# Kernel optimization log

Hardware: AMD Instinct MI355X
Metric: run time of the kernel (lower is better)

Reference implementation:

```python
import jax, jax.numpy as jnp
import numpy as np


def setup_inputs() -> dict:
    key = jax.random.key(0)
    ks = jax.random.split(key, 9)
    B, S, D, E, I = 4, 2048, 1024, 8, 2048
    sd = 1.0 / np.sqrt(D)
    si = 1.0 / np.sqrt(I)
    return {
        "hidden_states": jax.random.normal(ks[0], (B, S, D), dtype=jnp.float32),
        "gate_w": jax.random.normal(ks[1], (D, E), dtype=jnp.float32) * sd,
        "expert_gate_w": jax.random.normal(ks[2], (E, D, I), dtype=jnp.float32) * sd,
        "expert_up_w": jax.random.normal(ks[3], (E, D, I), dtype=jnp.float32) * sd,
        "expert_down_w": jax.random.normal(ks[4], (E, I, D), dtype=jnp.float32) * si,
        "shared_gate_proj_w": jax.random.normal(ks[5], (D, I), dtype=jnp.float32) * sd,
        "shared_up_w": jax.random.normal(ks[6], (D, I), dtype=jnp.float32) * sd,
        "shared_down_w": jax.random.normal(ks[7], (I, D), dtype=jnp.float32) * si,
        "shared_expert_gate_w": jax.random.normal(ks[8], (D, 1), dtype=jnp.float32) * sd,
        "top_k": 2,
    }


def reference(hidden_states, gate_w, expert_gate_w, expert_up_w, expert_down_w,
              shared_gate_proj_w, shared_up_w, shared_down_w, shared_expert_gate_w,
              top_k):
    B, S, D = hidden_states.shape
    E = gate_w.shape[1]
    x = hidden_states.reshape(-1, D)            # [T, D]
    T = x.shape[0]

    # Router: softmax in fp32, top-k, dense per-token per-expert combine weights.
    gate_vals = x @ gate_w                      # [T, E]
    probs = jax.nn.softmax(gate_vals.astype(jnp.float32), axis=-1)
    top_w, top_i = jax.lax.top_k(probs, top_k)  # [T, K]
    dense_w = jnp.zeros((T, E), dtype=jnp.float32)
    dense_w = dense_w.at[jnp.arange(T)[:, None], top_i].set(top_w)
    dense_w = dense_w.astype(x.dtype)           # zero for unselected experts

    # All experts as batched SwiGLU GEMMs (tokens with zero weight contribute 0).
    g = jnp.einsum('td,edi->eti', x, expert_gate_w)
    u = jnp.einsum('td,edi->eti', x, expert_up_w)
    y = jnp.einsum('eti,eid->etd', jax.nn.silu(g) * u, expert_down_w)  # [E, T, D]
    moe_out = jnp.einsum('etd,te->td', y, dense_w)                      # [T, D]

    # Shared expert with sigmoid gate.
    shared = (jax.nn.silu(x @ shared_gate_proj_w) * (x @ shared_up_w)) @ shared_down_w
    shared = jax.nn.sigmoid(x @ shared_expert_gate_w) * shared

    final = (moe_out + shared).reshape(B, S, D)
    return final, gate_vals
```

## Files before the change

kernel.cpp:

```cpp
#include <hip/hip_runtime.h>

typedef __bf16 bf16x8 __attribute__((ext_vector_type(8)));
typedef float f32x4 __attribute__((ext_vector_type(4)));
typedef float f4 __attribute__((ext_vector_type(4)));
typedef unsigned short us8 __attribute__((ext_vector_type(8)));

#define T_TOK 8192
#define DDIM 1024
#define NEXP 8
#define IDIM 2048
#define NCH 1024
#define RROWS 17408
#define ROWS_TOT (T_TOK + RROWS)

__device__ __forceinline__ unsigned short f2bf(float f) {
    unsigned u = __float_as_uint(f);
    u += 0x7fffu + ((u >> 16) & 1u);
    return (unsigned short)(u >> 16);
}

__global__ __launch_bounds__(256) void router_kernel(
    const float* __restrict__ x, const float* __restrict__ gate_w,
    const float* __restrict__ sgw, float* __restrict__ gate_out,
    float* __restrict__ wdense, float* __restrict__ sgout)
{
    __shared__ float lgw[DDIM * NEXP];
    __shared__ float lsg[DDIM];
    int tid = threadIdx.x;
    for (int i = tid; i < (DDIM * NEXP) / 4; i += 256)
        ((f4*)lgw)[i] = ((const f4*)gate_w)[i];
    for (int i = tid; i < DDIM / 4; i += 256)
        ((f4*)lsg)[i] = ((const f4*)sgw)[i];
    __syncthreads();

    int wid = tid >> 6, l = tid & 63;
    int t = blockIdx.x * 4 + wid;

    float acc[NEXP];
#pragma unroll
    for (int e = 0; e < NEXP; e++) acc[e] = 0.f;
    float accs = 0.f;
    const float* xr = x + (size_t)t * DDIM;
#pragma unroll
    for (int j = 0; j < 4; j++) {
        int d0 = j * 256 + l * 4;
        f4 xv = *(const f4*)(xr + d0);
#pragma unroll
        for (int c = 0; c < 4; c++) {
            float xd = xv[c];
            int d = d0 + c;
#pragma unroll
            for (int e = 0; e < NEXP; e++) acc[e] += xd * lgw[d * NEXP + e];
            accs += xd * lsg[d];
        }
    }
#pragma unroll
    for (int off = 32; off > 0; off >>= 1) {
#pragma unroll
        for (int e = 0; e < NEXP; e++) acc[e] += __shfl_xor(acc[e], off);
        accs += __shfl_xor(accs, off);
    }
    if (l == 0) {
        float m = acc[0];
        for (int e = 1; e < NEXP; e++) m = fmaxf(m, acc[e]);
        float p[NEXP], s = 0.f;
        for (int e = 0; e < NEXP; e++) { p[e] = __expf(acc[e] - m); s += p[e]; }
        float inv = 1.f / s;
        int i1 = 0; float b1 = p[0];
        for (int e = 1; e < NEXP; e++) if (p[e] > b1) { b1 = p[e]; i1 = e; }
        int i2 = -1; float b2 = -1.f;
        for (int e = 0; e < NEXP; e++) if (e != i1 && p[e] > b2) { b2 = p[e]; i2 = e; }
        for (int e = 0; e < NEXP; e++) {
            gate_out[(size_t)t * NEXP + e] = acc[e];
            float w = (e == i1) ? b1 * inv : (e == i2) ? b2 * inv : 0.f;
            wdense[(size_t)t * NEXP + e] = w;
        }
        sgout[t] = 1.f / (1.f + __expf(-accs));
    }
}

__global__ __launch_bounds__(256) void bucket_kernel(
    const float* __restrict__ wdense, int* __restrict__ list,
    float* __restrict__ wl, int* __restrict__ cnt,
    int* __restrict__ te, int* __restrict__ tp)
{
    int e = blockIdx.x;
    int tid = threadIdx.x, wid = tid >> 6, l = tid & 63;
    __shared__ int wsum[4];
    int base = 0;
    int* le = list + (size_t)e * T_TOK;
    float* we = wl + (size_t)e * T_TOK;
    for (int t0 = 0; t0 < T_TOK; t0 += 256) {
        int tok = t0 + tid;
        float w = wdense[(size_t)tok * NEXP + e];
        bool f = w > 0.f;
        unsigned long long m = __ballot(f);
        int lp = __popcll(m & ((1ull << l) - 1ull));
        if (l == 0) wsum[wid] = __popcll(m);
        __syncthreads();
        int woff = 0;
#pragma unroll
        for (int i = 0; i < 4; i++) if (i < wid) woff += wsum[i];
        int btot = wsum[0] + wsum[1] + wsum[2] + wsum[3];
        if (f) {
            int pos = base + woff + lp;
            le[pos] = tok; we[pos] = w;
            int slot = 0;
            for (int e2 = 0; e2 < e; e2++)
                slot += (wdense[(size_t)tok * NEXP + e2] > 0.f) ? 1 : 0;
            te[tok * 2 + slot] = e;
            tp[tok * 2 + slot] = pos;
        }
        base += btot;
        __syncthreads();
    }
    if (tid == 0) cnt[e] = base;
    int align = (base + 127) & ~127;
    for (int i = base + tid; i < align; i += 256) { le[i] = 0; we[i] = 0.f; }
}

__global__ void scan_kernel(const int* __restrict__ cnt, int* __restrict__ offs)
{
    if (threadIdx.x == 0) {
        int o = 0;
        for (int e = 0; e < NEXP; e++) { offs[e] = o; o += (cnt[e] + 127) & ~127; }
    }
}

__global__ __launch_bounds__(256) void cvt_kernel(
    const float* __restrict__ in, unsigned short* __restrict__ out, int n8)
{
    int i = blockIdx.x * 256 + threadIdx.x;
    if (i >= n8) return;
    const f4* p = (const f4*)in + (size_t)i * 2;
    f4 a = p[0], b = p[1];
    us8 o;
#pragma unroll
    for (int k = 0; k < 4; k++) { o[k] = f2bf(a[k]); o[4 + k] = f2bf(b[k]); }
    *((us8*)out + i) = o;
}

__global__ __launch_bounds__(256) void wcvt_gu_kernel(
    const float* __restrict__ egw, const float* __restrict__ euw,
    const float* __restrict__ sgp, const float* __restrict__ sup,
    unsigned short* __restrict__ pool, int c0)
{
    int j = blockIdx.y;
    int e = j >> 1, s = j & 1;
    const float* src = (e < 8) ? ((s ? euw : egw) + (size_t)e * DDIM * IDIM)
                               : (s ? sup : sgp);
    unsigned short* dst = pool + (size_t)j * NCH * DDIM;
    int tpc = NCH / 64;
    int tci = blockIdx.x % tpc, tri = blockIdx.x / tpc;
    int r0 = tri * 64;
    int cl0 = tci * 64;
    int cg0 = c0 + cl0;

    __shared__ unsigned short lds[64][72];
    int t = threadIdx.x;
    int tr = t >> 4, tcc = (t & 15) * 4;
#pragma unroll
    for (int jj = 0; jj < 4; jj++) {
        int r = tr + jj * 16;
        f4 v = *(const f4*)(src + (size_t)(r0 + r) * IDIM + cg0 + tcc);
#pragma unroll
        for (int k = 0; k < 4; k++) lds[r][tcc + k] = f2bf(v[k]);
    }
    __syncthreads();
    int orow = t >> 2, ss = t & 3;
    us8 v0, v1;
#pragma unroll
    for (int i = 0; i < 8; i++) {
        v0[i] = lds[ss * 16 + i][orow];
        v1[i] = lds[ss * 16 + 8 + i][orow];
    }
    unsigned short* op = dst + (size_t)(cl0 + orow) * DDIM + r0 + ss * 16;
    *(us8*)op = v0; *(us8*)(op + 8) = v1;
}

__global__ __launch_bounds__(256) void wcvt_d_kernel(
    const float* __restrict__ edw, const float* __restrict__ sdw,
    unsigned short* __restrict__ pool)
{
    int j = blockIdx.y;
    const float* src = (j < 8) ? edw + (size_t)j * IDIM * DDIM : sdw;
    unsigned short* dst = pool + (size_t)j * DDIM * IDIM;
    int tpc = DDIM / 64;
    int tci = blockIdx.x % tpc, tri = blockIdx.x / tpc;
    int rg0 = tri * 64;
    int cg0 = tci * 64;

    __shared__ unsigned short lds[64][72];
    int t = threadIdx.x;
    int tr = t >> 4, tcc = (t & 15) * 4;
#pragma unroll
    for (int jj = 0; jj < 4; jj++) {
        int r = tr + jj * 16;
        f4 v = *(const f4*)(src + (size_t)(rg0 + r) * DDIM + cg0 + tcc);
#pragma unroll
        for (int k = 0; k < 4; k++) lds[r][tcc + k] = f2bf(v[k]);
    }
    __syncthreads();
    int orow = t >> 2, ss = t & 3;
    us8 v0, v1;
#pragma unroll
    for (int i = 0; i < 8; i++) {
        v0[i] = lds[ss * 16 + i][orow];
        v1[i] = lds[ss * 16 + 8 + i][orow];
    }
    unsigned short* op = dst + (size_t)(cg0 + orow) * IDIM + rg0 + ss * 16;
    *(us8*)op = v0; *(us8*)(op + 8) = v1;
}

__device__ __forceinline__ void stage_tile(
    const unsigned short* __restrict__ g, int row0, int ldk, int k0,
    unsigned short* lds, int wid, int lane)
{
#pragma unroll
    for (int j = 0; j < 2; j++) {
        int c = wid + j * 4;
        int seg = c * 64 + lane;
        int row = seg >> 2, ks = seg & 3;
        const unsigned short* gp = g + (size_t)(row0 + row) * ldk + k0 + ks * 8;
        __builtin_amdgcn_global_load_lds(
            (const __attribute__((address_space(1))) void*)gp,
            (__attribute__((address_space(3))) void*)(lds + c * 512),
            16, 0, 0);
    }
}

__global__ __launch_bounds__(256, 2) void gemm_gateup(
    const unsigned short* __restrict__ A, const unsigned short* __restrict__ pool,
    unsigned short* __restrict__ H, const int* __restrict__ listb,
    const int* __restrict__ cnt, const int* __restrict__ offs, int c0)
{
    int z = blockIdx.z;
    const unsigned short *Bg, *Bu; const int* lst; int count, rowb;
    if (z == 0) {
        Bg = pool + (size_t)16 * NCH * DDIM; Bu = pool + (size_t)17 * NCH * DDIM;
        lst = nullptr; count = T_TOK; rowb = 0;
    } else {
        int e = z - 1;
        Bg = pool + (size_t)(e * 2) * NCH * DDIM; Bu = pool + (size_t)(e * 2 + 1) * NCH * DDIM;
        lst = listb + (size_t)e * T_TOK; count = cnt[e]; rowb = T_TOK + offs[e];
    }
    int flat = blockIdx.y * 8 + blockIdx.x;
    int nt = flat & 7, mt = flat >> 3;
    int m0 = mt * 128, n0 = nt * 128;
    if (m0 >= count) return;
    const int K = DDIM;

    __shared__ unsigned short As[128 * 32], Bgs[128 * 32], Bus[128 * 32];
    int tid = threadIdx.x, wid = tid >> 6, l = tid & 63;
    int wm = wid >> 1, wn = wid & 1;
    int lr = l & 15, kg = l >> 4;

    int seg0 = wid * 64 + l, seg1 = (wid + 4) * 64 + l;
    int ra0 = seg0 >> 2, ka0 = seg0 & 3;
    int ra1 = seg1 >> 2, ka1 = seg1 & 3;
    int ga0 = lst ? lst[m0 + ra0] : (m0 + ra0);
    int ga1 = lst ? lst[m0 + ra1] : (m0 + ra1);
    const unsigned short* pa0 = A + (size_t)ga0 * K + ka0 * 8;
    const unsigned short* pa1 = A + (size_t)ga1 * K + ka1 * 8;

    f32x4 zero = {0.f, 0.f, 0.f, 0.f};
    f32x4 accg[4][4], accu[4][4];
#pragma unroll
    for (int m = 0; m < 4; m++)
#pragma unroll
        for (int n = 0; n < 4; n++) { accg[m][n] = zero; accu[m][n] = zero; }

    for (int k0 = 0; k0 < K; k0 += 32) {
        __builtin_amdgcn_global_load_lds(
            (const __attribute__((address_space(1))) void*)(pa0 + k0),
            (__attribute__((address_space(3))) void*)(As + wid * 512), 16, 0, 0);
        __builtin_amdgcn_global_load_lds(
            (const __attribute__((address_space(1))) void*)(pa1 + k0),
            (__attribute__((address_space(3))) void*)(As + (wid + 4) * 512), 16, 0, 0);
        stage_tile(Bg, n0, K, k0, Bgs, wid, l);
        stage_tile(Bu, n0, K, k0, Bus, wid, l);
        __syncthreads();
        bf16x8 a[4], bg[4], bu[4];
#pragma unroll
        for (int m = 0; m < 4; m++)
            a[m] = *(const bf16x8*)(As + ((wm * 64 + m * 16 + lr) * 32 + kg * 8));
#pragma unroll
        for (int n = 0; n < 4; n++) {
            bg[n] = *(const bf16x8*)(Bgs + ((wn * 64 + n * 16 + lr) * 32 + kg * 8));
            bu[n] = *(const bf16x8*)(Bus + ((wn * 64 + n * 16 + lr) * 32 + kg * 8));
        }
#pragma unroll
        for (int m = 0; m < 4; m++)
#pragma unroll
            for (int n = 0; n < 4; n++) {
                accg[m][n] = __builtin_amdgcn_mfma_f32_16x16x32_bf16(a[m], bg[n], accg[m][n], 0, 0, 0);
                accu[m][n] = __builtin_amdgcn_mfma_f32_16x16x32_bf16(a[m], bu[n], accu[m][n], 0, 0, 0);
            }
        __syncthreads();
    }

#pragma unroll
    for (int m = 0; m < 4; m++) {
        int row = rowb + m0 + wm * 64 + m * 16 + kg * 4;
#pragma unroll
        for (int n = 0; n < 4; n++) {
            int col = c0 + n0 + wn * 64 + n * 16 + lr;
#pragma unroll
            for (int r = 0; r < 4; r++) {
                float g = accg[m][n][r], u = accu[m][n][r];
                float hv = g * (1.f / (1.f + __expf(-g))) * u;
                H[(size_t)(row + r) * IDIM + col] = f2bf(hv);
            }
        }
    }
}

__global__ __launch_bounds__(256, 2) void gemm_down(
    const unsigned short* __restrict__ H, const unsigned short* __restrict__ pool,
    unsigned short* __restrict__ Y,
    const float* __restrict__ wlb, const float* __restrict__ sgo,
    const int* __restrict__ cnt, const int* __restrict__ offs)
{
    int z = blockIdx.z;
    const unsigned short* B; const float* coef; int count, rowb;
    if (z == 0) {
        B = pool + (size_t)8 * DDIM * IDIM;
        coef = sgo; count = T_TOK; rowb = 0;
    } else {
        int e = z - 1;
        B = pool + (size_t)e * DDIM * IDIM;
        coef = wlb + (size_t)e * T_TOK;
        count = cnt[e]; rowb = T_TOK + offs[e];
    }
    int flat = blockIdx.y * 8 + blockIdx.x;
    int nt = flat & 7, mt = flat >> 3;
    int m0 = mt * 128, n0 = nt * 128;
    if (m0 >= count) return;
    const unsigned short* Arows = H + (size_t)rowb * IDIM;

    __shared__ unsigned short As[128 * 32], Bs[128 * 32];
    int tid = threadIdx.x, wid = tid >> 6, l = tid & 63;
    int wm = wid >> 1, wn = wid & 1;
    int lr = l & 15, kg = l >> 4;

    f32x4 zero = {0.f, 0.f, 0.f, 0.f};
    f32x4 acc[4][4];
#pragma unroll
    for (int m = 0; m < 4; m++)
#pragma unroll
        for (int n = 0; n < 4; n++) acc[m][n] = zero;

    for (int k0 = 0; k0 < IDIM; k0 += 32) {
        stage_tile(Arows, m0, IDIM, k0, As, wid, l);
        stage_tile(B, n0, IDIM, k0, Bs, wid, l);
        __syncthreads();
        bf16x8 a[4], b[4];
#pragma unroll
        for (int m = 0; m < 4; m++)
            a[m] = *(const bf16x8*)(As + ((wm * 64 + m * 16 + lr) * 32 + kg * 8));
#pragma unroll
        for (int n = 0; n < 4; n++)
            b[n] = *(const bf16x8*)(Bs + ((wn * 64 + n * 16 + lr) * 32 + kg * 8));
#pragma unroll
        for (int m = 0; m < 4; m++)
#pragma unroll
            for (int n = 0; n < 4; n++)
                acc[m][n] = __builtin_amdgcn_mfma_f32_16x16x32_bf16(a[m], b[n], acc[m][n], 0, 0, 0);
        __syncthreads();
    }

#pragma unroll
    for (int m = 0; m < 4; m++) {
        int rloc = m0 + wm * 64 + m * 16 + kg * 4;
        float cf[4];
#pragma unroll
        for (int r = 0; r < 4; r++) cf[r] = coef[rloc + r];
#pragma unroll
        for (int n = 0; n < 4; n++) {
            int col = n0 + wn * 64 + n * 16 + lr;
#pragma unroll
            for (int r = 0; r < 4; r++)
                Y[(size_t)(rowb + rloc + r) * DDIM + col] = f2bf(cf[r] * acc[m][n][r]);
        }
    }
}

__global__ __launch_bounds__(256) void combine_kernel(
    const unsigned short* __restrict__ Y, const int* __restrict__ te,
    const int* __restrict__ tp, const int* __restrict__ offs,
    float* __restrict__ out)
{
    int t = blockIdx.x * 2 + (threadIdx.x >> 7);
    int c = (threadIdx.x & 127) * 8;
    int e0 = te[2 * t], e1 = te[2 * t + 1];
    size_t r0 = (size_t)T_TOK + offs[e0] + tp[2 * t];
    size_t r1 = (size_t)T_TOK + offs[e1] + tp[2 * t + 1];

    us8 vs = *(const us8*)(Y + (size_t)t * DDIM + c);
    us8 v0 = *(const us8*)(Y + r0 * DDIM + c);
    us8 v1 = *(const us8*)(Y + r1 * DDIM + c);
    f4 o0, o1;
#pragma unroll
    for (int k = 0; k < 4; k++) {
        o0[k] = __uint_as_float((unsigned)vs[k] << 16)
              + __uint_as_float((unsigned)v0[k] << 16)
              + __uint_as_float((unsigned)v1[k] << 16);
        o1[k] = __uint_as_float((unsigned)vs[4 + k] << 16)
              + __uint_as_float((unsigned)v0[4 + k] << 16)
              + __uint_as_float((unsigned)v1[4 + k] << 16);
    }
    float* op = out + (size_t)t * DDIM + c;
    *(f4*)op = o0;
    *(f4*)(op + 4) = o1;
}

extern "C" void kernel_launch(void* const* d_in, const int* in_sizes, int n_in,
                              void* d_out, int out_size, void* d_ws, size_t ws_size,
                              hipStream_t stream)
{
    const float* x   = (const float*)d_in[0];
    const float* gw  = (const float*)d_in[1];
    const float* egw = (const float*)d_in[2];
    const float* euw = (const float*)d_in[3];
    const float* edw = (const float*)d_in[4];
    const float* sgp = (const float*)d_in[5];
    const float* sup = (const float*)d_in[6];
    const float* sdw = (const float*)d_in[7];
    const float* seg = (const float*)d_in[8];

    float* out0 = (float*)d_out;
    float* gate_out = out0 + (size_t)T_TOK * DDIM;

    char* ws = (char*)d_ws;
    auto take = [&](size_t bytes) { char* p = ws; ws += (bytes + 255) & ~(size_t)255; return p; };
    unsigned short* xb   = (unsigned short*)take((size_t)T_TOK * DDIM * 2);
    float* wdense = (float*)take((size_t)T_TOK * NEXP * 4);
    float* sgo    = (float*)take((size_t)T_TOK * 4);
    int*   list   = (int*)take((size_t)NEXP * T_TOK * 4);
    float* wl     = (float*)take((size_t)NEXP * T_TOK * 4);
    int*   cnt    = (int*)take(256);
    int*   offs   = (int*)take(256);
    int*   te     = (int*)take((size_t)T_TOK * 2 * 4);
    int*   tp     = (int*)take((size_t)T_TOK * 2 * 4);
    unsigned short* pool = (unsigned short*)take((size_t)18 * NCH * DDIM * 2);
    unsigned short* H    = (unsigned short*)take((size_t)ROWS_TOT * IDIM * 2);
    unsigned short* Y    = (unsigned short*)take((size_t)ROWS_TOT * DDIM * 2);

    router_kernel<<<T_TOK / 4, 256, 0, stream>>>(x, gw, seg, gate_out, wdense, sgo);
    bucket_kernel<<<NEXP, 256, 0, stream>>>(wdense, list, wl, cnt, te, tp);
    scan_kernel<<<1, 64, 0, stream>>>(cnt, offs);
    cvt_kernel<<<(T_TOK * DDIM / 8) / 256, 256, 0, stream>>>(x, xb, T_TOK * DDIM / 8);

    for (int c = 0; c < 2; c++) {
        int c0 = c * NCH;
        wcvt_gu_kernel<<<dim3((NCH / 64) * 16, 18), 256, 0, stream>>>(
            egw, euw, sgp, sup, pool, c0);
        gemm_gateup<<<dim3(8, 64, 9), 256, 0, stream>>>(
            xb, pool, H, list, cnt, offs, c0);
    }

    wcvt_d_kernel<<<dim3((IDIM / 64) * 16, 9), 256, 0, stream>>>(edw, sdw, pool);
    gemm_down<<<dim3(8, 64, 9), 256, 0, stream>>>(H, pool, Y, wl, sgo, cnt, offs);

    combine_kernel<<<T_TOK / 2, 256, 0, stream>>>(Y, te, tp, offs, out0);
}
```

Before: 590.8 us.

## Rewrite MoE GEMMs with 8-wave 256-row tiles, double-buffered swizzled LDS pipeline

Both the gate/up and down GEMMs move to 512-thread blocks with 256-row M tiles (down also uses 256-wide N) and K steps of 64. They use a two-stage double-buffered global-to-LDS pipeline with explicit vmcnt waits, XOR-swizzled LDS layout to avoid bank conflicts, interleaved MFMA phases with s_setprio, and split barriers. Expert bucket padding grows to 256 rows and stores are guarded to the 128-aligned count. The intent is to overlap memory with compute, raise arithmetic intensity, and cut LDS conflicts. The cost is more register and LDS pressure (64 KB per buffer pair) and wasted work on padded rows.

```diff
diff --git a/kernel.cpp b/kernel.cpp
--- a/kernel.cpp
+++ b/kernel.cpp
@@ -18,6 +18,10 @@
     u += 0x7fffu + ((u >> 16) & 1u);
     return (unsigned short)(u >> 16);
 }
+
+#define GLDS(src, dst) __builtin_amdgcn_global_load_lds( \
+    (const __attribute__((address_space(1))) void*)(src), \
+    (__attribute__((address_space(3))) void*)(dst), 16, 0, 0)
 
 __global__ __launch_bounds__(256) void router_kernel(
     const float* __restrict__ x, const float* __restrict__ gate_w,
@@ -115,7 +119,7 @@
         __syncthreads();
     }
     if (tid == 0) cnt[e] = base;
-    int align = (base + 127) & ~127;
+    int align = (base + 255) & ~255;
     for (int i = base + tid; i < align; i += 256) { le[i] = 0; we[i] = 0.f; }
 }
 
@@ -212,24 +216,7 @@
     *(us8*)op = v0; *(us8*)(op + 8) = v1;
 }
 
-__device__ __forceinline__ void stage_tile(
-    const unsigned short* __restrict__ g, int row0, int ldk, int k0,
-    unsigned short* lds, int wid, int lane)
-{
-#pragma unroll
-    for (int j = 0; j < 2; j++) {
-        int c = wid + j * 4;
-        int seg = c * 64 + lane;
-        int row = seg >> 2, ks = seg & 3;
-        const unsigned short* gp = g + (size_t)(row0 + row) * ldk + k0 + ks * 8;
-        __builtin_amdgcn_global_load_lds(
-            (const __attribute__((address_space(1))) void*)gp,
-            (__attribute__((address_space(3))) void*)(lds + c * 512),
-            16, 0, 0);
-    }
-}
-
-__global__ __launch_bounds__(256, 2) void gemm_gateup(
+__global__ __launch_bounds__(512, 2) void gemm_gateup8(
     const unsigned short* __restrict__ A, const unsigned short* __restrict__ pool,
     unsigned short* __restrict__ H, const int* __restrict__ listb,
     const int* __restrict__ cnt, const int* __restrict__ offs, int c0)
@@ -244,24 +231,60 @@
         Bg = pool + (size_t)(e * 2) * NCH * DDIM; Bu = pool + (size_t)(e * 2 + 1) * NCH * DDIM;
         lst = listb + (size_t)e * T_TOK; count = cnt[e]; rowb = T_TOK + offs[e];
     }
-    int flat = blockIdx.y * 8 + blockIdx.x;
-    int nt = flat & 7, mt = flat >> 3;
-    int m0 = mt * 128, n0 = nt * 128;
+    int m0 = blockIdx.y * 256, n0 = blockIdx.x * 128;
     if (m0 >= count) return;
-    const int K = DDIM;
-
-    __shared__ unsigned short As[128 * 32], Bgs[128 * 32], Bus[128 * 32];
+    int climit = (count + 127) & ~127;
+    const int NT = DDIM / 64;
+
+    __shared__ unsigned short lds[2][32768];
+
     int tid = threadIdx.x, wid = tid >> 6, l = tid & 63;
     int wm = wid >> 1, wn = wid & 1;
-    int lr = l & 15, kg = l >> 4;
-
-    int seg0 = wid * 64 + l, seg1 = (wid + 4) * 64 + l;
-    int ra0 = seg0 >> 2, ka0 = seg0 & 3;
-    int ra1 = seg1 >> 2, ka1 = seg1 & 3;
-    int ga0 = lst ? lst[m0 + ra0] : (m0 + ra0);
-    int ga1 = lst ? lst[m0 + ra1] : (m0 + ra1);
-    const unsigned short* pa0 = A + (size_t)ga0 * K + ka0 * 8;
-    const unsigned short* pa1 = A + (size_t)ga1 * K + ka1 * 8;
+    int lr = l & 15, lkg = l >> 4;
+
+    int sb = tid & 7, sr = tid >> 3;
+    int sk = (sb ^ (sr & 7)) << 3;
+    const unsigned short* pa[2][2];
+#pragma unroll
+    for (int h = 0; h < 2; h++)
+#pragma unroll
+        for (int j = 0; j < 2; j++) {
+            int rr = m0 + h * 128 + j * 64 + sr;
+            int ga = lst ? lst[rr] : rr;
+            pa[h][j] = A + (size_t)ga * DDIM + sk;
+        }
+    const unsigned short* pbg = Bg + (size_t)(n0 + sr) * DDIM + sk;
+    const unsigned short* pbu = Bu + (size_t)(n0 + sr) * DDIM + sk;
+
+#define GU_ST_A(sbuf, h, t) { \
+    GLDS(pa[h][0] + (t) * 64, (sbuf) + (h) * 8192 + tid * 8); \
+    GLDS(pa[h][1] + (t) * 64, (sbuf) + (h) * 8192 + 4096 + tid * 8); }
+#define GU_ST_BG(sbuf, t) { \
+    GLDS(pbg + (t) * 64, (sbuf) + 16384 + tid * 8); \
+    GLDS(pbg + (size_t)64 * DDIM + (t) * 64, (sbuf) + 16384 + 4096 + tid * 8); }
+#define GU_ST_BU(sbuf, t) { \
+    GLDS(pbu + (t) * 64, (sbuf) + 24576 + tid * 8); \
+    GLDS(pbu + (size_t)64 * DDIM + (t) * 64, (sbuf) + 24576 + 4096 + tid * 8); }
+
+    {
+        unsigned short* s0 = &lds[0][0];
+        GU_ST_A(s0, 0, 0); GU_ST_A(s0, 1, 0); GU_ST_BG(s0, 0); GU_ST_BU(s0, 0);
+        unsigned short* s1 = &lds[1][0];
+        GU_ST_A(s1, 0, 1); GU_ST_A(s1, 1, 1); GU_ST_BG(s1, 1); GU_ST_BU(s1, 1);
+    }
+
+    int xorc = (lr & 7) << 3;
+    int kx0 = (lkg * 8) ^ xorc;
+    int kx1 = (32 + lkg * 8) ^ xorc;
+    int aoff[4], boff[4];
+#pragma unroll
+    for (int mf = 0; mf < 4; mf++) {
+        int r = wm * 64 + mf * 16 + lr;
+        aoff[mf] = (r >> 7) * 8192 + (r & 127) * 64;
+    }
+#pragma unroll
+    for (int nf = 0; nf < 4; nf++)
+        boff[nf] = 16384 + (wn * 64 + nf * 16 + lr) * 64;
 
     f32x4 zero = {0.f, 0.f, 0.f, 0.f};
     f32x4 accg[4][4], accu[4][4];
@@ -270,52 +293,115 @@
 #pragma unroll
         for (int n = 0; n < 4; n++) { accg[m][n] = zero; accu[m][n] = zero; }
 
-    for (int k0 = 0; k0 < K; k0 += 32) {
-        __builtin_amdgcn_global_load_lds(
-            (const __attribute__((address_space(1))) void*)(pa0 + k0),
-            (__attribute__((address_space(3))) void*)(As + wid * 512), 16, 0, 0);
-        __builtin_amdgcn_global_load_lds(
-            (const __attribute__((address_space(1))) void*)(pa1 + k0),
-            (__attribute__((address_space(3))) void*)(As + (wid + 4) * 512), 16, 0, 0);
-        stage_tile(Bg, n0, K, k0, Bgs, wid, l);
-        stage_tile(Bu, n0, K, k0, Bus, wid, l);
-        __syncthreads();
-        bf16x8 a[4], bg[4], bu[4];
-#pragma unroll
-        for (int m = 0; m < 4; m++)
-            a[m] = *(const bf16x8*)(As + ((wm * 64 + m * 16 + lr) * 32 + kg * 8));
-#pragma unroll
-        for (int n = 0; n < 4; n++) {
-            bg[n] = *(const bf16x8*)(Bgs + ((wn * 64 + n * 16 + lr) * 32 + kg * 8));
-            bu[n] = *(const bf16x8*)(Bus + ((wn * 64 + n * 16 + lr) * 32 + kg * 8));
-        }
-#pragma unroll
-        for (int m = 0; m < 4; m++)
-#pragma unroll
-            for (int n = 0; n < 4; n++) {
-                accg[m][n] = __builtin_amdgcn_mfma_f32_16x16x32_bf16(a[m], bg[n], accg[m][n], 0, 0, 0);
-                accu[m][n] = __builtin_amdgcn_mfma_f32_16x16x32_bf16(a[m], bu[n], accu[m][n], 0, 0, 0);
+    bf16x8 a[2][2], bg[4][2], bu[4][2];
+
+#pragma unroll 1
+    for (int t = 0; t < NT; t++) {
+        const unsigned short* cb = &lds[t & 1][0];
+        unsigned short* sbuf = &lds[t & 1][0];
+        bool stg = (t + 2 < NT);
+
+        if (t == NT - 1) { asm volatile("s_waitcnt vmcnt(0)" ::: "memory"); }
+        else             { asm volatile("s_waitcnt vmcnt(8)" ::: "memory"); }
+        __builtin_amdgcn_s_barrier();
+#pragma unroll
+        for (int mf = 0; mf < 2; mf++) {
+            a[mf][0] = *(const bf16x8*)(cb + aoff[mf] + kx0);
+            a[mf][1] = *(const bf16x8*)(cb + aoff[mf] + kx1);
+        }
+#pragma unroll
+        for (int nf = 0; nf < 2; nf++) {
+            bg[nf][0] = *(const bf16x8*)(cb + boff[nf] + kx0);
+            bg[nf][1] = *(const bf16x8*)(cb + boff[nf] + kx1);
+            bu[nf][0] = *(const bf16x8*)(cb + boff[nf] + 8192 + kx0);
+            bu[nf][1] = *(const bf16x8*)(cb + boff[nf] + 8192 + kx1);
+        }
+        __builtin_amdgcn_s_setprio(1);
+#pragma unroll
+        for (int kh = 0; kh < 2; kh++)
+#pragma unroll
+            for (int mf = 0; mf < 2; mf++)
+#pragma unroll
+                for (int nf = 0; nf < 2; nf++) {
+                    accg[mf][nf] = __builtin_amdgcn_mfma_f32_16x16x32_bf16(a[mf][kh], bg[nf][kh], accg[mf][nf], 0, 0, 0);
+                    accu[mf][nf] = __builtin_amdgcn_mfma_f32_16x16x32_bf16(a[mf][kh], bu[nf][kh], accu[mf][nf], 0, 0, 0);
+                }
+        __builtin_amdgcn_s_setprio(0);
+
+        __builtin_amdgcn_s_barrier();
+#pragma unroll
+        for (int nf = 2; nf < 4; nf++) {
+            bg[nf][0] = *(const bf16x8*)(cb + boff[nf] + kx0);
+            bg[nf][1] = *(const bf16x8*)(cb + boff[nf] + kx1);
+            bu[nf][0] = *(const bf16x8*)(cb + boff[nf] + 8192 + kx0);
+            bu[nf][1] = *(const bf16x8*)(cb + boff[nf] + 8192 + kx1);
+        }
+        __builtin_amdgcn_s_setprio(1);
+#pragma unroll
+        for (int kh = 0; kh < 2; kh++)
+#pragma unroll
+            for (int mf = 0; mf < 2; mf++)
+#pragma unroll
+                for (int nf = 2; nf < 4; nf++) {
+                    accg[mf][nf] = __builtin_amdgcn_mfma_f32_16x16x32_bf16(a[mf][kh], bg[nf][kh], accg[mf][nf], 0, 0, 0);
+                    accu[mf][nf] = __builtin_amdgcn_mfma_f32_16x16x32_bf16(a[mf][kh], bu[nf][kh], accu[mf][nf], 0, 0, 0);
+                }
+        __builtin_amdgcn_s_setprio(0);
+
+        __builtin_amdgcn_s_barrier();
+#pragma unroll
+        for (int mf = 0; mf < 2; mf++) {
+            a[mf][0] = *(const bf16x8*)(cb + aoff[2 + mf] + kx0);
+            a[mf][1] = *(const bf16x8*)(cb + aoff[2 + mf] + kx1);
+        }
+        if (stg) { GU_ST_BG(sbuf, t + 2); }
+        __builtin_amdgcn_s_setprio(1);
+#pragma unroll
+        for (int kh = 0; kh < 2; kh++)
+#pragma unroll
+            for (int mf = 0; mf < 2; mf++)
+#pragma unroll
+                for (int nf = 0; nf < 2; nf++) {
+                    accg[2 + mf][nf] = __builtin_amdgcn_mfma_f32_16x16x32_bf16(a[mf][kh], bg[nf][kh], accg[2 + mf][nf], 0, 0, 0);
+                    accu[2 + mf][nf] = __builtin_amdgcn_mfma_f32_16x16x32_bf16(a[mf][kh], bu[nf][kh], accu[2 + mf][nf], 0, 0, 0);
+                }
+        __builtin_amdgcn_s_setprio(0);
+
+        __builtin_amdgcn_s_barrier();
+        if (stg) { GU_ST_BU(sbuf, t + 2); GU_ST_A(sbuf, 0, t + 2); GU_ST_A(sbuf, 1, t + 2); }
+        __builtin_amdgcn_s_setprio(1);
+#pragma unroll
+        for (int kh = 0; kh < 2; kh++)
+#pragma unroll
+            for (int mf = 0; mf < 2; mf++)
+#pragma unroll
+                for (int nf = 2; nf < 4; nf++) {
+                    accg[2 + mf][nf] = __builtin_amdgcn_mfma_f32_16x16x32_bf16(a[mf][kh], bg[nf][kh], accg[2 + mf][nf], 0, 0, 0);
+                    accu[2 + mf][nf] = __builtin_amdgcn_mfma_f32_16x16x32_bf16(a[mf][kh], bu[nf][kh], accu[2 + mf][nf], 0, 0, 0);
+                }
+        __builtin_amdgcn_s_setprio(0);
+    }
+
+#pragma unroll
+    for (int mf = 0; mf < 4; mf++) {
+        int rbase = m0 + wm * 64 + mf * 16 + lkg * 4;
+#pragma unroll
+        for (int nf = 0; nf < 4; nf++) {
+            int col = c0 + n0 + wn * 64 + nf * 16 + lr;
+#pragma unroll
+            for (int r = 0; r < 4; r++) {
+                int rloc = rbase + r;
+                if (rloc < climit) {
+                    float g = accg[mf][nf][r], u = accu[mf][nf][r];
+                    float hv = g * (1.f / (1.f + __expf(-g))) * u;
+                    H[(size_t)(rowb + rloc) * IDIM + col] = f2bf(hv);
+                }
             }
-        __syncthreads();
-    }
-
-#pragma unroll
-    for (int m = 0; m < 4; m++) {
-        int row = rowb + m0 + wm * 64 + m * 16 + kg * 4;
-#pragma unroll
-        for (int n = 0; n < 4; n++) {
-            int col = c0 + n0 + wn * 64 + n * 16 + lr;
-#pragma unroll
-            for (int r = 0; r < 4; r++) {
-                float g = accg[m][n][r], u = accu[m][n][r];
-                float hv = g * (1.f / (1.f + __expf(-g))) * u;
-                H[(size_t)(row + r) * IDIM + col] = f2bf(hv);
-            }
-        }
-    }
-}
-
-__global__ __launch_bounds__(256, 2) void gemm_down(
+        }
+    }
+}
+
+__global__ __launch_bounds__(512, 2) void gemm_down8(
     const unsigned short* __restrict__ H, const unsigned short* __restrict__ pool,
     unsigned short* __restrict__ Y,
     const float* __restrict__ wlb, const float* __restrict__ sgo,
@@ -332,55 +418,149 @@
         coef = wlb + (size_t)e * T_TOK;
         count = cnt[e]; rowb = T_TOK + offs[e];
     }
-    int flat = blockIdx.y * 8 + blockIdx.x;
-    int nt = flat & 7, mt = flat >> 3;
-    int m0 = mt * 128, n0 = nt * 128;
+    int m0 = blockIdx.y * 256, n0 = blockIdx.x * 256;
     if (m0 >= count) return;
-    const unsigned short* Arows = H + (size_t)rowb * IDIM;
-
-    __shared__ unsigned short As[128 * 32], Bs[128 * 32];
+    int climit = (count + 127) & ~127;
+    const int NT = IDIM / 64;
+
+    __shared__ unsigned short lds[2][32768];
+
     int tid = threadIdx.x, wid = tid >> 6, l = tid & 63;
-    int wm = wid >> 1, wn = wid & 1;
-    int lr = l & 15, kg = l >> 4;
+    int wm = wid >> 2, wn = wid & 3;
+    int lr = l & 15, lkg = l >> 4;
+
+    int sb = tid & 7, sr = tid >> 3;
+    int sk = (sb ^ (sr & 7)) << 3;
+    const unsigned short* pah = H + (size_t)(rowb + m0 + sr) * IDIM + sk;
+    const unsigned short* pb  = B + (size_t)(n0 + sr) * IDIM + sk;
+
+#define DN_ST_A(sbuf, h, t) { \
+    GLDS(pah + (size_t)((h) * 128) * IDIM + (t) * 64, (sbuf) + (h) * 8192 + tid * 8); \
+    GLDS(pah + (size_t)((h) * 128 + 64) * IDIM + (t) * 64, (sbuf) + (h) * 8192 + 4096 + tid * 8); }
+#define DN_ST_B(sbuf, h, t) { \
+    GLDS(pb + (size_t)((h) * 128) * IDIM + (t) * 64, (sbuf) + 16384 + (h) * 8192 + tid * 8); \
+    GLDS(pb + (size_t)((h) * 128 + 64) * IDIM + (t) * 64, (sbuf) + 16384 + (h) * 8192 + 4096 + tid * 8); }
+
+    {
+        unsigned short* s0 = &lds[0][0];
+        DN_ST_A(s0, 0, 0); DN_ST_A(s0, 1, 0); DN_ST_B(s0, 0, 0); DN_ST_B(s0, 1, 0);
+        unsigned short* s1 = &lds[1][0];
+        DN_ST_A(s1, 0, 1); DN_ST_A(s1, 1, 1); DN_ST_B(s1, 0, 1); DN_ST_B(s1, 1, 1);
+    }
+
+    int xorc = (lr & 7) << 3;
+    int kx0 = (lkg * 8) ^ xorc;
+    int kx1 = (32 + lkg * 8) ^ xorc;
+    int aoff[8], boff[4];
+#pragma unroll
+    for (int mf = 0; mf < 8; mf++)
+        aoff[mf] = wm * 8192 + (mf * 16 + lr) * 64;
+#pragma unroll
+    for (int nf = 0; nf < 4; nf++)
+        boff[nf] = 16384 + (wn * 64 + nf * 16 + lr) * 64;
 
     f32x4 zero = {0.f, 0.f, 0.f, 0.f};
-    f32x4 acc[4][4];
-#pragma unroll
-    for (int m = 0; m < 4; m++)
+    f32x4 acc[8][4];
+#pragma unroll
+    for (int m = 0; m < 8; m++)
 #pragma unroll
         for (int n = 0; n < 4; n++) acc[m][n] = zero;
 
-    for (int k0 = 0; k0 < IDIM; k0 += 32) {
-        stage_tile(Arows, m0, IDIM, k0, As, wid, l);
-        stage_tile(B, n0, IDIM, k0, Bs, wid, l);
-        __syncthreads();
-        bf16x8 a[4], b[4];
-#pragma unroll
-        for (int m = 0; m < 4; m++)
-            a[m] = *(const bf16x8*)(As + ((wm * 64 + m * 16 + lr) * 32 + kg * 8));
-#pragma unroll
-        for (int n = 0; n < 4; n++)
-            b[n] = *(const bf16x8*)(Bs + ((wn * 64 + n * 16 + lr) * 32 + kg * 8));
-#pragma unroll
-        for (int m = 0; m < 4; m++)
-#pragma unroll
-            for (int n = 0; n < 4; n++)
-                acc[m][n] = __builtin_amdgcn_mfma_f32_16x16x32_bf16(a[m], b[n], acc[m][n], 0, 0, 0);
-        __syncthreads();
-    }
-
-#pragma unroll
-    for (int m = 0; m < 4; m++) {
-        int rloc = m0 + wm * 64 + m * 16 + kg * 4;
+    bf16x8 a[4][2], b[4][2];
+
+#pragma unroll 1
+    for (int t = 0; t < NT; t++) {
+        const unsigned short* cb = &lds[t & 1][0];
+        unsigned short* sbuf = &lds[t & 1][0];
+        bool stg = (t + 2 < NT);
+
+        if (t == NT - 1) { asm volatile("s_waitcnt vmcnt(0)" ::: "memory"); }
+        else             { asm volatile("s_waitcnt vmcnt(8)" ::: "memory"); }
+        __builtin_amdgcn_s_barrier();
+#pragma unroll
+        for (int mf = 0; mf < 4; mf++) {
+            a[mf][0] = *(const bf16x8*)(cb + aoff[mf] + kx0);
+            a[mf][1] = *(const bf16x8*)(cb + aoff[mf] + kx1);
+        }
+#pragma unroll
+        for (int nf = 0; nf < 2; nf++) {
+            b[nf][0] = *(const bf16x8*)(cb + boff[nf] + kx0);
+            b[nf][1] = *(const bf16x8*)(cb + boff[nf] + kx1);
+        }
+        __builtin_amdgcn_s_setprio(1);
+#pragma unroll
+        for (int kh = 0; kh < 2; kh++)
+#pragma unroll
+            for (int mf = 0; mf < 4; mf++)
+#pragma unroll
+                for (int nf = 0; nf < 2; nf++)
+                    acc[mf][nf] = __builtin_amdgcn_mfma_f32_16x16x32_bf16(a[mf][kh], b[nf][kh], acc[mf][nf], 0, 0, 0);
+        __builtin_amdgcn_s_setprio(0);
+
+        __builtin_amdgcn_s_barrier();
+#pragma unroll
+        for (int nf = 2; nf < 4; nf++) {
+            b[nf][0] = *(const bf16x8*)(cb + boff[nf] + kx0);
+            b[nf][1] = *(const bf16x8*)(cb + boff[nf] + kx1);
+        }
+        __builtin_amdgcn_s_setprio(1);
+#pragma unroll
+        for (int kh = 0; kh < 2; kh++)
+#pragma unroll
+            for (int mf = 0; mf < 4; mf++)
+#pragma unroll
+                for (int nf = 2; nf < 4; nf++)
+                    acc[mf][nf] = __builtin_amdgcn_mfma_f32_16x16x32_bf16(a[mf][kh], b[nf][kh], acc[mf][nf], 0, 0, 0);
+        __builtin_amdgcn_s_setprio(0);
+
+        __builtin_amdgcn_s_barrier();
+#pragma unroll
+        for (int mf = 0; mf < 4; mf++) {
+            a[mf][0] = *(const bf16x8*)(cb + aoff[4 + mf] + kx0);
+            a[mf][1] = *(const bf16x8*)(cb + aoff[4 + mf] + kx1);
+        }
+        if (stg) { DN_ST_B(sbuf, 0, t + 2); }
+        __builtin_amdgcn_s_setprio(1);
+#pragma unroll
+        for (int kh = 0; kh < 2; kh++)
+#pragma unroll
+            for (int mf = 0; mf < 4; mf++)
+#pragma unroll
+                for (int nf = 0; nf < 2; nf++)
+                    acc[4 + mf][nf] = __builtin_amdgcn_mfma_f32_16x16x32_bf16(a[mf][kh], b[nf][kh], acc[4 + mf][nf], 0, 0, 0);
+        __builtin_amdgcn_s_setprio(0);
+
+        __builtin_amdgcn_s_barrier();
+        if (stg) { DN_ST_B(sbuf, 1, t + 2); DN_ST_A(sbuf, 0, t + 2); DN_ST_A(sbuf, 1, t + 2); }
+        __builtin_amdgcn_s_setprio(1);
+#pragma unroll
+        for (int kh = 0; kh < 2; kh++)
+#pragma unroll
+            for (int mf = 0; mf < 4; mf++)
+#pragma unroll
+                for (int nf = 2; nf < 4; nf++)
+                    acc[4 + mf][nf] = __builtin_amdgcn_mfma_f32_16x16x32_bf16(a[mf][kh], b[nf][kh], acc[4 + mf][nf], 0, 0, 0);
+        __builtin_amdgcn_s_setprio(0);
+    }
+
+#pragma unroll
+    for (int mf = 0; mf < 8; mf++) {
+        int rbase = m0 + wm * 128 + mf * 16 + lkg * 4;
         float cf[4];
 #pragma unroll
-        for (int r = 0; r < 4; r++) cf[r] = coef[rloc + r];
-#pragma unroll
-        for (int n = 0; n < 4; n++) {
-            int col = n0 + wn * 64 + n * 16 + lr;
-#pragma unroll
-            for (int r = 0; r < 4; r++)
-                Y[(size_t)(rowb + rloc + r) * DDIM + col] = f2bf(cf[r] * acc[m][n][r]);
+        for (int r = 0; r < 4; r++) {
+            int rloc = rbase + r;
+            cf[r] = (rloc < climit) ? coef[rloc] : 0.f;
+        }
+#pragma unroll
+        for (int nf = 0; nf < 4; nf++) {
+            int col = n0 + wn * 64 + nf * 16 + lr;
+#pragma unroll
+            for (int r = 0; r < 4; r++) {
+                int rloc = rbase + r;
+                if (rloc < climit)
+                    Y[(size_t)(rowb + rloc) * DDIM + col] = f2bf(cf[r] * acc[mf][nf][r]);
+            }
         }
     }
 }
@@ -455,12 +635,13 @@
         int c0 = c * NCH;
         wcvt_gu_kernel<<<dim3((NCH / 64) * 16, 18), 256, 0, stream>>>(
             egw, euw, sgp, sup, pool, c0);
-        gemm_gateup<<<dim3(8, 64, 9), 256, 0, stream>>>(
+        gemm_gateup8<<<dim3(NCH / 128, T_TOK / 256, 9), 512, 0, stream>>>(
             xb, pool, H, list, cnt, offs, c0);
     }
 
     wcvt_d_kernel<<<dim3((IDIM / 64) * 16, 9), 256, 0, stream>>>(edw, sdw, pool);
-    gemm_down<<<dim3(8, 64, 9), 256, 0, stream>>>(H, pool, Y, wl, sgo, cnt, offs);
+    gemm_down8<<<dim3(DDIM / 256, T_TOK / 256, 9), 512, 0, stream>>>(
+        H, pool, Y, wl, sgo, cnt, offs);
 
     combine_kernel<<<T_TOK / 2, 256, 0, stream>>>(Y, te, tp, offs, out0);
 }
```

After: 552.0 us. -6.6%, faster.

## Double-buffer GEMM LDS staging with XOR-swizzled layout and prefetch depth two

Applied to the files above, without the earlier changes.

Rewrites both expert GEMMs to use a two-stage LDS ring filled by direct global-to-LDS loads issued two K-tiles ahead, synchronized with explicit vmcnt waits and raw barriers. It also applies an XOR swizzle to the K offset so the bf16x8 LDS reads avoid bank conflicts. Launch bounds for the down GEMM go up to 4 blocks per CU, and the bucket padding changes from 128 to 256 rows with guarded epilogue stores. The goal is to overlap global loads with MFMA work and cut LDS conflicts, at the cost of more shared memory per block and fragile hand-managed wait counts.

```diff
diff --git a/kernel.cpp b/kernel.cpp
--- a/kernel.cpp
+++ b/kernel.cpp
@@ -18,6 +18,10 @@
     u += 0x7fffu + ((u >> 16) & 1u);
     return (unsigned short)(u >> 16);
 }
+
+#define GLDS(src, dst) __builtin_amdgcn_global_load_lds( \
+    (const __attribute__((address_space(1))) void*)(src), \
+    (__attribute__((address_space(3))) void*)(dst), 16, 0, 0)
 
 __global__ __launch_bounds__(256) void router_kernel(
     const float* __restrict__ x, const float* __restrict__ gate_w,
@@ -115,7 +119,7 @@
         __syncthreads();
     }
     if (tid == 0) cnt[e] = base;
-    int align = (base + 127) & ~127;
+    int align = (base + 255) & ~255;
     for (int i = base + tid; i < align; i += 256) { le[i] = 0; we[i] = 0.f; }
 }
 
@@ -212,24 +216,8 @@
     *(us8*)op = v0; *(us8*)(op + 8) = v1;
 }
 
-__device__ __forceinline__ void stage_tile(
-    const unsigned short* __restrict__ g, int row0, int ldk, int k0,
-    unsigned short* lds, int wid, int lane)
-{
-#pragma unroll
-    for (int j = 0; j < 2; j++) {
-        int c = wid + j * 4;
-        int seg = c * 64 + lane;
-        int row = seg >> 2, ks = seg & 3;
-        const unsigned short* gp = g + (size_t)(row0 + row) * ldk + k0 + ks * 8;
-        __builtin_amdgcn_global_load_lds(
-            (const __attribute__((address_space(1))) void*)gp,
-            (__attribute__((address_space(3))) void*)(lds + c * 512),
-            16, 0, 0);
-    }
-}
-
-__global__ __launch_bounds__(256, 2) void gemm_gateup(
+
+__global__ __launch_bounds__(256, 2) void gemm_gateup8(
     const unsigned short* __restrict__ A, const unsigned short* __restrict__ pool,
     unsigned short* __restrict__ H, const int* __restrict__ listb,
     const int* __restrict__ cnt, const int* __restrict__ offs, int c0)
@@ -244,24 +232,49 @@
         Bg = pool + (size_t)(e * 2) * NCH * DDIM; Bu = pool + (size_t)(e * 2 + 1) * NCH * DDIM;
         lst = listb + (size_t)e * T_TOK; count = cnt[e]; rowb = T_TOK + offs[e];
     }
-    int flat = blockIdx.y * 8 + blockIdx.x;
-    int nt = flat & 7, mt = flat >> 3;
-    int m0 = mt * 128, n0 = nt * 128;
+    int m0 = blockIdx.y * 128, n0 = blockIdx.x * 128;
     if (m0 >= count) return;
-    const int K = DDIM;
-
-    __shared__ unsigned short As[128 * 32], Bgs[128 * 32], Bus[128 * 32];
+    int climit = (count + 127) & ~127;
+    const int NT = DDIM / 32;
+
+    __shared__ unsigned short lds[2][12288];
+
     int tid = threadIdx.x, wid = tid >> 6, l = tid & 63;
     int wm = wid >> 1, wn = wid & 1;
-    int lr = l & 15, kg = l >> 4;
-
-    int seg0 = wid * 64 + l, seg1 = (wid + 4) * 64 + l;
-    int ra0 = seg0 >> 2, ka0 = seg0 & 3;
-    int ra1 = seg1 >> 2, ka1 = seg1 & 3;
-    int ga0 = lst ? lst[m0 + ra0] : (m0 + ra0);
-    int ga1 = lst ? lst[m0 + ra1] : (m0 + ra1);
-    const unsigned short* pa0 = A + (size_t)ga0 * K + ka0 * 8;
-    const unsigned short* pa1 = A + (size_t)ga1 * K + ka1 * 8;
+    int lr = l & 15, lkg = l >> 4;
+
+    int srow0 = tid >> 2, srow1 = 64 + (tid >> 2);
+    int skof = (((tid & 3) ^ ((tid >> 3) & 3))) << 3;
+    int ga0 = lst ? lst[m0 + srow0] : (m0 + srow0);
+    int ga1 = lst ? lst[m0 + srow1] : (m0 + srow1);
+    const unsigned short* paA0 = A + (size_t)ga0 * DDIM + skof;
+    const unsigned short* paA1 = A + (size_t)ga1 * DDIM + skof;
+    const unsigned short* pbg0 = Bg + (size_t)(n0 + srow0) * DDIM + skof;
+    const unsigned short* pbg1 = Bg + (size_t)(n0 + srow1) * DDIM + skof;
+    const unsigned short* pbu0 = Bu + (size_t)(n0 + srow0) * DDIM + skof;
+    const unsigned short* pbu1 = Bu + (size_t)(n0 + srow1) * DDIM + skof;
+
+#define GU_ST(sbuf, t) { \
+    GLDS(paA0 + (t) * 32, (sbuf) + tid * 8); \
+    GLDS(paA1 + (t) * 32, (sbuf) + 2048 + tid * 8); \
+    GLDS(pbg0 + (t) * 32, (sbuf) + 4096 + tid * 8); \
+    GLDS(pbg1 + (t) * 32, (sbuf) + 6144 + tid * 8); \
+    GLDS(pbu0 + (t) * 32, (sbuf) + 8192 + tid * 8); \
+    GLDS(pbu1 + (t) * 32, (sbuf) + 10240 + tid * 8); }
+
+    GU_ST(&lds[0][0], 0);
+    GU_ST(&lds[1][0], 1);
+    asm volatile("s_waitcnt vmcnt(6)" ::: "memory");
+    __builtin_amdgcn_s_barrier();
+
+    int kx = ((lkg) ^ ((lr >> 1) & 3)) << 3;
+    int aoff[4], goff[4], uoff[4];
+#pragma unroll
+    for (int f = 0; f < 4; f++) {
+        aoff[f] = (wm * 64 + f * 16 + lr) * 32 + kx;
+        goff[f] = 4096 + (wn * 64 + f * 16 + lr) * 32 + kx;
+        uoff[f] = 8192 + (wn * 64 + f * 16 + lr) * 32 + kx;
+    }
 
     f32x4 zero = {0.f, 0.f, 0.f, 0.f};
     f32x4 accg[4][4], accu[4][4];
@@ -270,52 +283,55 @@
 #pragma unroll
         for (int n = 0; n < 4; n++) { accg[m][n] = zero; accu[m][n] = zero; }
 
-    for (int k0 = 0; k0 < K; k0 += 32) {
-        __builtin_amdgcn_global_load_lds(
-            (const __attribute__((address_space(1))) void*)(pa0 + k0),
-            (__attribute__((address_space(3))) void*)(As + wid * 512), 16, 0, 0);
-        __builtin_amdgcn_global_load_lds(
-            (const __attribute__((address_space(1))) void*)(pa1 + k0),
-            (__attribute__((address_space(3))) void*)(As + (wid + 4) * 512), 16, 0, 0);
-        stage_tile(Bg, n0, K, k0, Bgs, wid, l);
-        stage_tile(Bu, n0, K, k0, Bus, wid, l);
-        __syncthreads();
+    for (int t = 0; t < NT; t++) {
+        const unsigned short* cb = &lds[t & 1][0];
+        unsigned short* sbuf = &lds[t & 1][0];
+        bool stg = (t + 2 < NT);
+
         bf16x8 a[4], bg[4], bu[4];
 #pragma unroll
-        for (int m = 0; m < 4; m++)
-            a[m] = *(const bf16x8*)(As + ((wm * 64 + m * 16 + lr) * 32 + kg * 8));
-#pragma unroll
-        for (int n = 0; n < 4; n++) {
-            bg[n] = *(const bf16x8*)(Bgs + ((wn * 64 + n * 16 + lr) * 32 + kg * 8));
-            bu[n] = *(const bf16x8*)(Bus + ((wn * 64 + n * 16 + lr) * 32 + kg * 8));
-        }
-#pragma unroll
-        for (int m = 0; m < 4; m++)
-#pragma unroll
-            for (int n = 0; n < 4; n++) {
-                accg[m][n] = __builtin_amdgcn_mfma_f32_16x16x32_bf16(a[m], bg[n], accg[m][n], 0, 0, 0);
-                accu[m][n] = __builtin_amdgcn_mfma_f32_16x16x32_bf16(a[m], bu[n], accu[m][n], 0, 0, 0);
+        for (int f = 0; f < 4; f++) {
+            a[f]  = *(const bf16x8*)(cb + aoff[f]);
+            bg[f] = *(const bf16x8*)(cb + goff[f]);
+            bu[f] = *(const bf16x8*)(cb + uoff[f]);
+        }
+#pragma unroll
+        for (int mf = 0; mf < 4; mf++)
+#pragma unroll
+            for (int nf = 0; nf < 4; nf++) {
+                accg[mf][nf] = __builtin_amdgcn_mfma_f32_16x16x32_bf16(a[mf], bg[nf], accg[mf][nf], 0, 0, 0);
+                accu[mf][nf] = __builtin_amdgcn_mfma_f32_16x16x32_bf16(a[mf], bu[nf], accu[mf][nf], 0, 0, 0);
             }
-        __syncthreads();
-    }
-
-#pragma unroll
-    for (int m = 0; m < 4; m++) {
-        int row = rowb + m0 + wm * 64 + m * 16 + kg * 4;
-#pragma unroll
-        for (int n = 0; n < 4; n++) {
-            int col = c0 + n0 + wn * 64 + n * 16 + lr;
+        __builtin_amdgcn_s_barrier();
+        if (stg) {
+            GU_ST(sbuf, t + 2);
+            asm volatile("s_waitcnt vmcnt(6)" ::: "memory");
+        } else {
+            asm volatile("s_waitcnt vmcnt(0)" ::: "memory");
+        }
+        __builtin_amdgcn_s_barrier();
+    }
+
+#pragma unroll
+    for (int mf = 0; mf < 4; mf++) {
+        int rbase = m0 + wm * 64 + mf * 16 + lkg * 4;
+#pragma unroll
+        for (int nf = 0; nf < 4; nf++) {
+            int col = c0 + n0 + wn * 64 + nf * 16 + lr;
 #pragma unroll
             for (int r = 0; r < 4; r++) {
-                float g = accg[m][n][r], u = accu[m][n][r];
-                float hv = g * (1.f / (1.f + __expf(-g))) * u;
-                H[(size_t)(row + r) * IDIM + col] = f2bf(hv);
+                int rloc = rbase + r;
+                if (rloc < climit) {
+                    float g = accg[mf][nf][r], u = accu[mf][nf][r];
+                    float hv = g * (1.f / (1.f + __expf(-g))) * u;
+                    H[(size_t)(rowb + rloc) * IDIM + col] = f2bf(hv);
+                }
             }
         }
     }
 }
 
-__global__ __launch_bounds__(256, 2) void gemm_down(
+__global__ __launch_bounds__(256, 4) void gemm_down8(
     const unsigned short* __restrict__ H, const unsigned short* __restrict__ pool,
     unsigned short* __restrict__ Y,
     const float* __restrict__ wlb, const float* __restrict__ sgo,
@@ -332,16 +348,42 @@
         coef = wlb + (size_t)e * T_TOK;
         count = cnt[e]; rowb = T_TOK + offs[e];
     }
-    int flat = blockIdx.y * 8 + blockIdx.x;
-    int nt = flat & 7, mt = flat >> 3;
-    int m0 = mt * 128, n0 = nt * 128;
+    int m0 = blockIdx.y * 128, n0 = blockIdx.x * 128;
     if (m0 >= count) return;
-    const unsigned short* Arows = H + (size_t)rowb * IDIM;
-
-    __shared__ unsigned short As[128 * 32], Bs[128 * 32];
+    int climit = (count + 127) & ~127;
+    const int NT = IDIM / 32;
+
+    __shared__ unsigned short lds[2][8192];
+
     int tid = threadIdx.x, wid = tid >> 6, l = tid & 63;
     int wm = wid >> 1, wn = wid & 1;
-    int lr = l & 15, kg = l >> 4;
+    int lr = l & 15, lkg = l >> 4;
+
+    int srow0 = tid >> 2, srow1 = 64 + (tid >> 2);
+    int skof = (((tid & 3) ^ ((tid >> 3) & 3))) << 3;
+    const unsigned short* paH0 = H + (size_t)(rowb + m0 + srow0) * IDIM + skof;
+    const unsigned short* paH1 = H + (size_t)(rowb + m0 + srow1) * IDIM + skof;
+    const unsigned short* pbB0 = B + (size_t)(n0 + srow0) * IDIM + skof;
+    const unsigned short* pbB1 = B + (size_t)(n0 + srow1) * IDIM + skof;
+
+#define DN_ST(sbuf, t) { \
+    GLDS(paH0 + (t) * 32, (sbuf) + tid * 8); \
+    GLDS(paH1 + (t) * 32, (sbuf) + 2048 + tid * 8); \
+    GLDS(pbB0 + (t) * 32, (sbuf) + 4096 + tid * 8); \
+    GLDS(pbB1 + (t) * 32, (sbuf) + 6144 + tid * 8); }
+
+    DN_ST(&lds[0][0], 0);
+    DN_ST(&lds[1][0], 1);
+    asm volatile("s_waitcnt vmcnt(4)" ::: "memory");
+    __builtin_amdgcn_s_barrier();
+
+    int kx = ((lkg) ^ ((lr >> 1) & 3)) << 3;
+    int aoff[4], boff[4];
+#pragma unroll
+    for (int f = 0; f < 4; f++) {
+        aoff[f] = (wm * 64 + f * 16 + lr) * 32 + kx;
+        boff[f] = 4096 + (wn * 64 + f * 16 + lr) * 32 + kx;
+    }
 
     f32x4 zero = {0.f, 0.f, 0.f, 0.f};
     f32x4 acc[4][4];
@@ -350,37 +392,50 @@
 #pragma unroll
         for (int n = 0; n < 4; n++) acc[m][n] = zero;
 
-    for (int k0 = 0; k0 < IDIM; k0 += 32) {
-        stage_tile(Arows, m0, IDIM, k0, As, wid, l);
-        stage_tile(B, n0, IDIM, k0, Bs, wid, l);
-        __syncthreads();
+    for (int t = 0; t < NT; t++) {
+        const unsigned short* cb = &lds[t & 1][0];
+        unsigned short* sbuf = &lds[t & 1][0];
+        bool stg = (t + 2 < NT);
+
         bf16x8 a[4], b[4];
 #pragma unroll
-        for (int m = 0; m < 4; m++)
-            a[m] = *(const bf16x8*)(As + ((wm * 64 + m * 16 + lr) * 32 + kg * 8));
-#pragma unroll
-        for (int n = 0; n < 4; n++)
-            b[n] = *(const bf16x8*)(Bs + ((wn * 64 + n * 16 + lr) * 32 + kg * 8));
-#pragma unroll
-        for (int m = 0; m < 4; m++)
-#pragma unroll
-            for (int n = 0; n < 4; n++)
-                acc[m][n] = __builtin_amdgcn_mfma_f32_16x16x32_bf16(a[m], b[n], acc[m][n], 0, 0, 0);
-        __syncthreads();
-    }
-
-#pragma unroll
-    for (int m = 0; m < 4; m++) {
-        int rloc = m0 + wm * 64 + m * 16 + kg * 4;
+        for (int f = 0; f < 4; f++) {
+            a[f] = *(const bf16x8*)(cb + aoff[f]);
+            b[f] = *(const bf16x8*)(cb + boff[f]);
+        }
+#pragma unroll
+        for (int mf = 0; mf < 4; mf++)
+#pragma unroll
+            for (int nf = 0; nf < 4; nf++)
+                acc[mf][nf] = __builtin_amdgcn_mfma_f32_16x16x32_bf16(a[mf], b[nf], acc[mf][nf], 0, 0, 0);
+        __builtin_amdgcn_s_barrier();
+        if (stg) {
+            DN_ST(sbuf, t + 2);
+            asm volatile("s_waitcnt vmcnt(4)" ::: "memory");
+        } else {
+            asm volatile("s_waitcnt vmcnt(0)" ::: "memory");
+        }
+        __builtin_amdgcn_s_barrier();
+    }
+
+#pragma unroll
+    for (int mf = 0; mf < 4; mf++) {
+        int rbase = m0 + wm * 64 + mf * 16 + lkg * 4;
         float cf[4];
 #pragma unroll
-        for (int r = 0; r < 4; r++) cf[r] = coef[rloc + r];
-#pragma unroll
-        for (int n = 0; n < 4; n++) {
-            int col = n0 + wn * 64 + n * 16 + lr;
-#pragma unroll
-            for (int r = 0; r < 4; r++)
-                Y[(size_t)(rowb + rloc + r) * DDIM + col] = f2bf(cf[r] * acc[m][n][r]);
+        for (int r = 0; r < 4; r++) {
+            int rloc = rbase + r;
+            cf[r] = (rloc < climit) ? coef[rloc] : 0.f;
+        }
+#pragma unroll
+        for (int nf = 0; nf < 4; nf++) {
+            int col = n0 + wn * 64 + nf * 16 + lr;
+#pragma unroll
+            for (int r = 0; r < 4; r++) {
+                int rloc = rbase + r;
+                if (rloc < climit)
+                    Y[(size_t)(rowb + rloc) * DDIM + col] = f2bf(cf[r] * acc[mf][nf][r]);
+            }
         }
     }
 }
@@ -455,12 +510,13 @@
         int c0 = c * NCH;
         wcvt_gu_kernel<<<dim3((NCH / 64) * 16, 18), 256, 0, stream>>>(
             egw, euw, sgp, sup, pool, c0);
-        gemm_gateup<<<dim3(8, 64, 9), 256, 0, stream>>>(
+        gemm_gateup8<<<dim3(NCH / 128, T_TOK / 128, 9), 256, 0, stream>>>(
             xb, pool, H, list, cnt, offs, c0);
     }
 
     wcvt_d_kernel<<<dim3((IDIM / 64) * 16, 9), 256, 0, stream>>>(edw, sdw, pool);
-    gemm_down<<<dim3(8, 64, 9), 256, 0, stream>>>(H, pool, Y, wl, sgo, cnt, offs);
+    gemm_down8<<<dim3(DDIM / 128, T_TOK / 128, 9), 256, 0, stream>>>(
+        H, pool, Y, wl, sgo, cnt, offs);
 
     combine_kernel<<<T_TOK / 2, 256, 0, stream>>>(Y, te, tp, offs, out0);
 }
```

Result: faster. 570.4 us (-3.5%).
